# Kernel tuning notes

Hardware: AMD Instinct MI355X
Metric: run time of the kernel (lower is better)

Reference implementation:

```python
import jax, jax.numpy as jnp
import numpy as np

NUM_BITS = 8
QMIN = -(2.0 ** (NUM_BITS - 1)) + 1.0   # -127
QMAX = 2.0 ** (NUM_BITS - 1) - 1.0      # 127
RUN_MIN, RUN_MAX = -1.0, 1.0            # eval-mode running_min/running_max buffers
KERNEL, STRIDE, PAD = 3, 1, 1

# input scale (concrete, from running stats): scale = max(|min|,|max|)/qmax, snapped to power of 2
_scale_in = max(max(abs(RUN_MAX), abs(RUN_MIN)) / QMAX, 1e-8)
INPUT_SCALE = float(2.0 ** np.round(np.log2(_scale_in)))  # 2^-7


def _ste_quant(x, scale):
    """shift (x/scale), clamp to [QMIN,QMAX], round; straight-through grad = 1/scale."""
    xs = x / scale
    return xs + jax.lax.stop_gradient(jnp.round(jnp.clip(xs, QMIN, QMAX)) - xs)


def _weight_scale(w):
    s = jnp.maximum(jnp.maximum(jnp.abs(jnp.max(w)), jnp.abs(jnp.min(w))) / QMAX, 1e-8)
    return 2.0 ** jnp.round(jnp.log2(s))


def _adder2d(qx, qw):
    """AdderNet SAD conv: out[n,f,i,j] = -sum_{c,kh,kw} |patch - w|."""
    N = qx.shape[0]
    Cout = qw.shape[0]
    patches = jax.lax.conv_general_dilated_patches(
        qx, (KERNEL, KERNEL), (STRIDE, STRIDE), [(PAD, PAD), (PAD, PAD)])
    _, K, Ho, Wo = patches.shape            # K = Cin*k*k, channel-major like OIHW reshape
    pr = patches.reshape(N, K, Ho * Wo)
    wf = qw.reshape(Cout, K)

    def per_out(wk):                         # wk: [K]
        return -jnp.sum(jnp.abs(pr - wk[None, :, None]), axis=1)  # [N, Ho*Wo]

    out = jax.lax.map(jax.checkpoint(per_out), wf)   # [Cout, N, Ho*Wo], sequential over Cout
    return jnp.transpose(out, (1, 0, 2)).reshape(N, Cout, Ho, Wo)


def reference(x, weight):
    # quantize input (eval mode, running stats scale = 2^-7)
    qx = _ste_quant(x, INPUT_SCALE)
    # quantize weight at its own power-of-2 scale (scale_index < 0 branch)
    s_w = jax.lax.stop_gradient(_weight_scale(weight))
    qw = _ste_quant(weight, s_w)
    # integer-domain SAD convolution
    q_out = _adder2d(qx, qw)
    # dequantize: round, clamp to int32 range, shift right by |scale_index| (== * INPUT_SCALE);
    # straight-through grad = INPUT_SCALE
    ys = q_out * INPUT_SCALE
    deq = jnp.clip(jnp.round(q_out), -2.0 ** 31 + 1, 2.0 ** 31 - 1) * INPUT_SCALE
    return ys + jax.lax.stop_gradient(deq - ys)


def setup_inputs() -> dict:
    key = jax.random.key(0)
    kx, kw = jax.random.split(key)
    x = jax.random.normal(kx, (16, 32, 128, 128), dtype=jnp.float32)
    weight = jax.random.normal(kw, (32, 32, 3, 3), dtype=jnp.float32)
    return {"x": x, "weight": weight}
```

## Files before the change

kernel.cpp:

```cpp
#include <hip/hip_runtime.h>
#include <stdint.h>

#define INPUT_SCALE 0.0078125f

__device__ __forceinline__ uint32_t sadu8(uint32_t a, uint32_t b, uint32_t c) {
#if __has_builtin(__builtin_amdgcn_sad_u8)
    return __builtin_amdgcn_sad_u8(a, b, c);
#else
    uint32_t d;
    asm("v_sad_u8 %0, %1, %2, %3" : "=v"(d) : "v"(a), "v"(b), "v"(c));
    return d;
#endif
}

__device__ __forceinline__ uint32_t qbyte(float x) {
    float v = fminf(fmaxf(x * 128.0f, -127.0f), 127.0f);
    return (uint32_t)((int)rintf(v) + 128);
}

__global__ __launch_bounds__(1024) void quant_weight(const float* __restrict__ w,
                                                     uint32_t* __restrict__ qwp) {
    __shared__ float red[1024];
    __shared__ float s_inv;
    int tid = threadIdx.x;
    float m = 0.0f;
    for (int i = tid; i < 9216; i += 1024) m = fmaxf(m, fabsf(w[i]));
    red[tid] = m;
    __syncthreads();
    for (int s = 512; s > 0; s >>= 1) {
        if (tid < s) red[tid] = fmaxf(red[tid], red[tid + s]);
        __syncthreads();
    }
    if (tid == 0) {
        float s = fmaxf(red[0] / 127.0f, 1e-8f);
        int e; float fr = frexpf(s, &e);
        int k = (fr >= 0.70710678118654752f) ? e : e - 1;
        s_inv = exp2f((float)(-k));
    }
    __syncthreads();
    float inv = s_inv;
    for (int u = tid; u < 2304; u += 1024) {
        int f = u / 72, rem = u % 72, kpos = rem / 8, cg = rem % 8;
        int kh = kpos / 3, kw = kpos % 3;
        uint32_t pk = 0;
        #pragma unroll
        for (int b = 0; b < 4; ++b) {
            int c = cg * 4 + b;
            float v = w[((f * 32 + c) * 3 + kh) * 3 + kw] * inv;
            v = fminf(fmaxf(v, -127.0f), 127.0f);
            pk |= ((uint32_t)((int)rintf(v) + 128) & 0xFFu) << (8 * b);
        }
        qwp[u] = pk;
    }
}

#define LSTRIDE 12
__global__ __launch_bounds__(512, 4) void adder_conv_fused(const float* __restrict__ x,
                                                           const uint32_t* __restrict__ qwp,
                                                           float* __restrict__ out) {
    __shared__ __align__(16) uint32_t sx[18 * 34 * LSTRIDE];
    int tid = threadIdx.x;
    int b = blockIdx.x;
    int n = b >> 5;
    int rem = b & 31;
    int h0 = (rem >> 2) * 16, w0 = (rem & 3) * 32;

    for (int q = tid; q < 4896; q += 512) {
        int cg = q / 612;
        int pixel = q - cg * 612;
        int r = pixel / 34, cc = pixel - r * 34;
        int gh = h0 - 1 + r, gw = w0 - 1 + cc;
        uint32_t pk = 0x80808080u;
        if ((unsigned)gh < 128u && (unsigned)gw < 128u) {
            const float* base = x + (((size_t)n * 32 + cg * 4) * 128 + gh) * 128 + gw;
            pk = qbyte(base[0])
               | (qbyte(base[16384]) << 8)
               | (qbyte(base[32768]) << 16)
               | (qbyte(base[49152]) << 24);
        }
        sx[pixel * LSTRIDE + cg] = pk;
    }
    __syncthreads();

    int c = tid & 31;
    int r = tid >> 5;

    uint4 qx[3][3][2];
    #pragma unroll
    for (int dr = 0; dr < 3; ++dr)
        #pragma unroll
        for (int dc = 0; dc < 3; ++dc) {
            const uint4* p = (const uint4*)(sx + ((r + dr) * 34 + (c + dc)) * LSTRIDE);
            qx[dr][dc][0] = p[0];
            qx[dr][dc][1] = p[1];
        }

    size_t obase = ((size_t)(n * 32) * 128 + (h0 + r)) * 128 + (w0 + c);
    #pragma unroll 2
    for (int f = 0; f < 32; ++f) {
        const uint32_t* wf = qwp + f * 72;
        uint32_t s0 = 0, s1 = 0, s2 = 0, s3 = 0;
        #pragma unroll
        for (int t = 0; t < 9; ++t) {
            int kh = t / 3, kw = t - kh * 3;
            uint4 wv0 = *(const uint4*)(wf + t * 8);
            uint4 wv1 = *(const uint4*)(wf + t * 8 + 4);
            uint4 x0 = qx[kh][kw][0], x1 = qx[kh][kw][1];
            s0 = sadu8(x0.x, wv0.x, s0);
            s1 = sadu8(x0.y, wv0.y, s1);
            s2 = sadu8(x0.z, wv0.z, s2);
            s3 = sadu8(x0.w, wv0.w, s3);
            s0 = sadu8(x1.x, wv1.x, s0);
            s1 = sadu8(x1.y, wv1.y, s1);
            s2 = sadu8(x1.z, wv1.z, s2);
            s3 = sadu8(x1.w, wv1.w, s3);
        }
        out[obase + (size_t)f * 16384] = -(float)((s0 + s1) + (s2 + s3)) * INPUT_SCALE;
    }
}

extern "C" void kernel_launch(void* const* d_in, const int* in_sizes, int n_in,
                              void* d_out, int out_size, void* d_ws, size_t ws_size,
                              hipStream_t stream) {
    const float* x = (const float*)d_in[0];
    const float* w = (const float*)d_in[1];
    float* out = (float*)d_out;

    uint32_t* qwp = (uint32_t*)d_ws;

    quant_weight<<<1, 1024, 0, stream>>>(w, qwp);
    adder_conv_fused<<<512, 512, 0, stream>>>(x, qwp, out);
}
```

Baseline: 48.39 us.

## Split output filters across half-blocks and halve spatial tile height

Each block now covers 8 rows instead of 16, and its two 256-thread halves each compute 16 of the 32 filters for the same pixels. Each thread loops taps outermost with 16 filter accumulators, instead of holding all nine input taps in registers. The grid doubles to 1024 blocks and the occupancy hint rises to 8 blocks per CU, aiming for more parallelism and latency hiding. In exchange, the halo load overhead per output pixel grows with the shorter tile, and the shared-memory input is read twice, once per filter half.

```diff
diff --git a/kernel.cpp b/kernel.cpp
--- a/kernel.cpp
+++ b/kernel.cpp
@@ -55,19 +55,19 @@
 }
 
 #define LSTRIDE 12
-__global__ __launch_bounds__(512, 4) void adder_conv_fused(const float* __restrict__ x,
+__global__ __launch_bounds__(512, 8) void adder_conv_fused(const float* __restrict__ x,
                                                            const uint32_t* __restrict__ qwp,
                                                            float* __restrict__ out) {
-    __shared__ __align__(16) uint32_t sx[18 * 34 * LSTRIDE];
+    __shared__ __align__(16) uint32_t sx[10 * 34 * LSTRIDE];
     int tid = threadIdx.x;
     int b = blockIdx.x;
-    int n = b >> 5;
-    int rem = b & 31;
-    int h0 = (rem >> 2) * 16, w0 = (rem & 3) * 32;
+    int n = b >> 6;
+    int rem = b & 63;
+    int h0 = (rem >> 2) * 8, w0 = (rem & 3) * 32;
 
-    for (int q = tid; q < 4896; q += 512) {
-        int cg = q / 612;
-        int pixel = q - cg * 612;
+    for (int q = tid; q < 2720; q += 512) {
+        int cg = q / 340;
+        int pixel = q - cg * 340;
         int r = pixel / 34, cc = pixel - r * 34;
         int gh = h0 - 1 + r, gw = w0 - 1 + cc;
         uint32_t pk = 0x80808080u;
@@ -82,40 +82,44 @@
     }
     __syncthreads();
 
-    int c = tid & 31;
-    int r = tid >> 5;
+    int fh = tid >> 8;
+    int px = tid & 255;
+    int r = px >> 5;
+    int c = px & 31;
 
-    uint4 qx[3][3][2];
+    const uint32_t* wfb = qwp + fh * 16 * 72;
+    uint32_t acc[16];
     #pragma unroll
-    for (int dr = 0; dr < 3; ++dr)
+    for (int f = 0; f < 16; ++f) acc[f] = 0u;
+
+    int lbase = (r * 34 + c) * LSTRIDE;
+    #pragma unroll
+    for (int t = 0; t < 9; ++t) {
+        int kh = t / 3, kw = t - kh * 3;
+        const uint4* p = (const uint4*)(sx + lbase + (kh * 34 + kw) * LSTRIDE);
+        uint4 x0 = p[0];
+        uint4 x1 = p[1];
         #pragma unroll
-        for (int dc = 0; dc < 3; ++dc) {
-            const uint4* p = (const uint4*)(sx + ((r + dr) * 34 + (c + dc)) * LSTRIDE);
-            qx[dr][dc][0] = p[0];
-            qx[dr][dc][1] = p[1];
+        for (int f = 0; f < 16; ++f) {
+            const uint4* wp = (const uint4*)(wfb + (f * 9 + t) * 8);
+            uint4 wv0 = wp[0], wv1 = wp[1];
+            uint32_t a = acc[f];
+            a = sadu8(x0.x, wv0.x, a);
+            a = sadu8(x0.y, wv0.y, a);
+            a = sadu8(x0.z, wv0.z, a);
+            a = sadu8(x0.w, wv0.w, a);
+            a = sadu8(x1.x, wv1.x, a);
+            a = sadu8(x1.y, wv1.y, a);
+            a = sadu8(x1.z, wv1.z, a);
+            a = sadu8(x1.w, wv1.w, a);
+            acc[f] = a;
         }
+    }
 
-    size_t obase = ((size_t)(n * 32) * 128 + (h0 + r)) * 128 + (w0 + c);
-    #pragma unroll 2
-    for (int f = 0; f < 32; ++f) {
-        const uint32_t* wf = qwp + f * 72;
-        uint32_t s0 = 0, s1 = 0, s2 = 0, s3 = 0;
-        #pragma unroll
-        for (int t = 0; t < 9; ++t) {
-            int kh = t / 3, kw = t - kh * 3;
-            uint4 wv0 = *(const uint4*)(wf + t * 8);
-            uint4 wv1 = *(const uint4*)(wf + t * 8 + 4);
-            uint4 x0 = qx[kh][kw][0], x1 = qx[kh][kw][1];
-            s0 = sadu8(x0.x, wv0.x, s0);
-            s1 = sadu8(x0.y, wv0.y, s1);
-            s2 = sadu8(x0.z, wv0.z, s2);
-            s3 = sadu8(x0.w, wv0.w, s3);
-            s0 = sadu8(x1.x, wv1.x, s0);
-            s1 = sadu8(x1.y, wv1.y, s1);
-            s2 = sadu8(x1.z, wv1.z, s2);
-            s3 = sadu8(x1.w, wv1.w, s3);
-        }
-        out[obase + (size_t)f * 16384] = -(float)((s0 + s1) + (s2 + s3)) * INPUT_SCALE;
+    size_t obase = (((size_t)n * 32 + fh * 16) * 128 + (h0 + r)) * 128 + (w0 + c);
+    #pragma unroll
+    for (int f = 0; f < 16; ++f) {
+        out[obase + (size_t)f * 16384] = -(float)acc[f] * INPUT_SCALE;
     }
 }
 
@@ -129,5 +133,5 @@
     uint32_t* qwp = (uint32_t*)d_ws;
 
     quant_weight<<<1, 1024, 0, stream>>>(w, qwp);
-    adder_conv_fused<<<512, 512, 0, stream>>>(x, qwp, out);
+    adder_conv_fused<<<1024, 512, 0, stream>>>(x, qwp, out);
 }
```

Result: slower. 107.3 us (+121.8%).
